# Kernel optimization log

Hardware: AMD Instinct MI355X
Metric: run time of the kernel (lower is better)

## Reference

```python
import jax, jax.numpy as jnp
import numpy as np
from jax import lax

H, HD, P, C, HID = 8, 64, 16, 512, 2048
ALIBI_ALPHA, START_I = 1.0, 0
EPS = 1e-5

def setup_inputs():
    key = jax.random.key(0)
    ks = jax.random.split(key, 20)
    s = 0.02
    return {
        "x": jax.random.normal(ks[0], (8, 1024, C), jnp.float32),
        "Wq": jax.random.normal(ks[1], (HD, HD), jnp.float32) * s,
        "Wk": jax.random.normal(ks[2], (HD, HD), jnp.float32) * s,
        "Wv": jax.random.normal(ks[3], (HD, HD), jnp.float32) * s,
        "Wo": jax.random.normal(ks[4], (C, C), jnp.float32) * s,
        "bo": jnp.zeros((C,), jnp.float32),
        "th_pre": jax.random.normal(ks[5], (H, H), jnp.float32) * (1.0 / np.sqrt(H)),
        "th_post": jax.random.normal(ks[6], (H, H), jnp.float32) * (1.0 / np.sqrt(H)),
        "p_keys": jax.random.normal(ks[7], (P, 1, HD), jnp.float32) * s,
        "p_values": jax.random.normal(ks[8], (P, 1, HD), jnp.float32) * s,
        "conv1_w": jax.random.normal(ks[9], (2 * HID, C, 3), jnp.float32) * s,
        "conv1_b": jnp.zeros((2 * HID,), jnp.float32),
        "conv2_w": jax.random.normal(ks[10], (C, HID, 3), jnp.float32) * s,
        "conv2_b": jnp.zeros((C,), jnp.float32),
        "ln1_g": jnp.ones((C,), jnp.float32),
        "ln1_b": jnp.zeros((C,), jnp.float32),
        "ln2_g": jnp.ones((C,), jnp.float32),
        "ln2_b": jnp.zeros((C,), jnp.float32),
    }

def _layernorm(x, g, b):
    mu = jnp.mean(x, axis=-1, keepdims=True)
    var = jnp.mean((x - mu) ** 2, axis=-1, keepdims=True)
    return (x - mu) * lax.rsqrt(var + EPS) * g + b

def _mha(x, Wq, Wk, Wv, Wo, bo, th_pre, th_post, p_keys, p_values):
    N, L, _ = x.shape
    xh = x.reshape(N, L, H, HD)
    q = xh @ Wq.T  # per-head-dim linear, as in torch (applied to last dim)
    k = xh @ Wk.T
    v = xh @ Wv.T
    # persistent memory: [P,1,HD] broadcast over batch and heads
    pk = jnp.broadcast_to(p_keys[None], (N, P, H, HD))
    pv = jnp.broadcast_to(p_values[None], (N, P, H, HD))
    k = jnp.concatenate([k, pk], axis=1)  # (N, L+P, H, HD)
    v = jnp.concatenate([v, pv], axis=1)
    energy = jnp.einsum('nqhd,nkhd->nhqk', q, k)
    # ALiBi: slope_h = 2^(-alpha*(h+1+start_i)), bias = -|q-k|*slope, zero on persistent cols
    slopes = 2.0 ** (-ALIBI_ALPHA * (jnp.arange(1, H + 1, dtype=jnp.float32) + START_I))
    t = jnp.arange(L, dtype=jnp.float32)
    dist = jnp.abs(t[:, None] - t[None, :])  # (L, L)
    bias = -dist[None, :, :] * slopes[:, None, None]  # (H, L, L)
    bias = jnp.pad(bias, ((0, 0), (0, 0), (0, P)))
    energy = energy + bias[None]
    energy = jnp.einsum('gh,nhqk->ngqk', th_pre, energy)  # pre-softmax talking heads (1x1 conv)
    attn = jax.nn.softmax(energy / jnp.sqrt(jnp.float32(C)), axis=-1)
    attn = jnp.einsum('gh,nhqk->ngqk', th_post, attn)  # post-softmax talking heads
    out = jnp.einsum('nhql,nlhd->nqhd', attn, v).reshape(N, L, C)
    return out @ Wo.T + bo

def _ffn(x, conv1_w, conv1_b, conv2_w, conv2_b):
    dn = ('NCH', 'OIH', 'NCH')
    xc = jnp.transpose(x, (0, 2, 1))  # (N, C, L)
    xp = jnp.pad(xc, ((0, 0), (0, 0), (1, 1)))  # same padding, k=3
    h = lax.conv_general_dilated(xp, conv1_w, (1,), 'VALID', dimension_numbers=dn) + conv1_b[None, :, None]
    h1, h2 = jnp.split(h, 2, axis=1)
    h = jax.nn.silu(h1) * h2  # swiglu
    hp = jnp.pad(h, ((0, 0), (0, 0), (1, 1)))
    y = lax.conv_general_dilated(hp, conv2_w, (1,), 'VALID', dimension_numbers=dn) + conv2_b[None, :, None]
    return jnp.transpose(y, (0, 2, 1))

def reference(x, Wq, Wk, Wv, Wo, bo, th_pre, th_post, p_keys, p_values,
              conv1_w, conv1_b, conv2_w, conv2_b, ln1_g, ln1_b, ln2_g, ln2_b):
    a = _mha(x, Wq, Wk, Wv, Wo, bo, th_pre, th_post, p_keys, p_values)
    x1 = _layernorm(a + x, ln1_g, ln1_b)
    f = _ffn(x1, conv1_w, conv1_b, conv2_w, conv2_b)
    return _layernorm(f + x1, ln2_g, ln2_b)
```

## Files before the change

kernel.cpp:

```cpp
#include <hip/hip_runtime.h>
#include <cstddef>
#include <cstdint>

#define NB   8
#define LQ   1024
#define CH   512
#define HHE  8
#define HDD  64
#define PPM  16
#define LP   1040
#define HID  2048

typedef unsigned short ushort_t;
typedef __attribute__((ext_vector_type(8))) short short8;
typedef __attribute__((ext_vector_type(4))) float floatx4;

static const size_t O_QB   = 0;
static const size_t O_KB   = 2097152;
static const size_t O_VB   = 4227072;
static const size_t O_VT   = 6356992;
static const size_t O_AOB  = 8486912;
static const size_t O_AF   = 10584064;
static const size_t O_X1B  = 16777216;
static const size_t O_HPAD = 18878464;
static const size_t O_W1   = 27283456;
static const size_t O_W2   = 30429184;
static const size_t O_WO   = 32002048;

__device__ __forceinline__ ushort_t f2bf(float f) {
  uint32_t u = __float_as_uint(f);
  u += 0x7FFFu + ((u >> 16) & 1u);
  return (ushort_t)(u >> 16);
}
__device__ __forceinline__ float bf2f(ushort_t h) {
  return __uint_as_float(((uint32_t)h) << 16);
}

__device__ __forceinline__ void async16(ushort_t* lds, const ushort_t* g) {
  __builtin_amdgcn_global_load_lds(
      (const __attribute__((address_space(1))) void*)g,
      (__attribute__((address_space(3))) void*)lds, 16, 0, 0);
}

__global__ __launch_bounds__(256) void pack_bf16_kernel(
    const float* __restrict__ src, ushort_t* __restrict__ dst,
    int K, int KD, int icShift)
{
  const int oc = blockIdx.x;
  const int icMask = (1 << icShift) - 1;
  for (int k = threadIdx.x; k < K; k += 256) {
    int ic = k & icMask, dl = k >> icShift;
    dst[(size_t)oc * K + k] = f2bf(src[(size_t)oc * K + ic * KD + dl]);
  }
}

template<int EPI>
__global__ __launch_bounds__(256, 2) void mfma_gemm(
    const ushort_t* __restrict__ Ab, const ushort_t* __restrict__ Bb,
    int K, int BS, int P, int NOUT,
    const float* __restrict__ bias, const float* __restrict__ res,
    float* __restrict__ outf, ushort_t* __restrict__ outh)
{
  __shared__ ushort_t As[128 * 32];
  __shared__ ushort_t Bs[128 * 32];
  const int t = threadIdx.x;
  const int w = t >> 6, l = t & 63;
  const int m0 = blockIdx.x * 128, n0 = blockIdx.y * 128;

  const int sub = l >> 2;
  const int kc8 = (l & 3) * 8;
  const ushort_t* aptr[2];
  const ushort_t* bptr[2];
  #pragma unroll
  for (int c = 0; c < 2; ++c) {
    int arow = m0 + w * 32 + c * 16 + sub;
    aptr[c] = Ab + (size_t)(arow >> 10) * BS + (size_t)(arow & 1023) * P + kc8;
    int brow = n0 + w * 32 + c * 16 + sub;
    bptr[c] = Bb + (size_t)brow * K + kc8;
  }

  const int wm = w >> 1, wn = w & 1;
  const int lm = l & 15, q = l >> 4;
  floatx4 acc[4][4];
  #pragma unroll
  for (int i = 0; i < 4; ++i)
    #pragma unroll
    for (int j = 0; j < 4; ++j)
      acc[i][j] = (floatx4){0.f, 0.f, 0.f, 0.f};

  const int kIters = K >> 5;
  for (int kt = 0; kt < kIters; ++kt) {
    __syncthreads();
    async16(&As[w * 1024 +   0], aptr[0]);
    async16(&As[w * 1024 + 512], aptr[1]);
    async16(&Bs[w * 1024 +   0], bptr[0]);
    async16(&Bs[w * 1024 + 512], bptr[1]);
    aptr[0] += 32; aptr[1] += 32; bptr[0] += 32; bptr[1] += 32;
    __syncthreads();
    short8 af[4], bf[4];
    #pragma unroll
    for (int i = 0; i < 4; ++i)
      af[i] = *(const short8*)&As[(wm * 64 + i * 16 + lm) * 32 + q * 8];
    #pragma unroll
    for (int i = 0; i < 4; ++i)
      bf[i] = *(const short8*)&Bs[(wn * 64 + i * 16 + lm) * 32 + q * 8];
    #pragma unroll
    for (int i = 0; i < 4; ++i)
      #pragma unroll
      for (int j = 0; j < 4; ++j)
        acc[i][j] = __builtin_amdgcn_mfma_f32_16x16x32_bf16(af[i], bf[j], acc[i][j], 0, 0, 0);
  }

  #pragma unroll
  for (int i = 0; i < 4; ++i) {
    #pragma unroll
    for (int j = 0; j < 4; ++j) {
      const int mbase = m0 + wm * 64 + i * 16 + q * 4;
      const int n = n0 + wn * 64 + j * 16 + lm;
      #pragma unroll
      for (int r = 0; r < 4; ++r) {
        const int m = mbase + r;
        float v = acc[i][j][r];
        if (EPI == 0) {
          outh[(size_t)m * NOUT + n] = f2bf(v);
        } else if (EPI == 1) {
          outf[(size_t)m * NOUT + n] = v + bias[n];
        } else {
          outf[(size_t)m * NOUT + n] = v + bias[n] + res[(size_t)m * NOUT + n];
        }
      }
    }
  }
}

__global__ __launch_bounds__(256) void qkv_mfma(
    const float* __restrict__ x,
    const float* __restrict__ Wq, const float* __restrict__ Wk, const float* __restrict__ Wv,
    ushort_t* __restrict__ qo, ushort_t* __restrict__ ko, ushort_t* __restrict__ vo)
{
  __shared__ ushort_t Ws[8 * 512];
  const int mat = blockIdx.y;
  const float* __restrict__ W = (mat == 0) ? Wq : (mat == 1) ? Wk : Wv;
  const int t = threadIdx.x;

  for (int e = t; e < 4096; e += 256) {
    const int oc = e >> 6, ic = e & 63;
    const int nt = oc >> 4, lmm = oc & 15, s = ic >> 5, qd = (ic >> 3) & 3, j = ic & 7;
    Ws[(((nt * 2 + s) * 4 + qd) * 16 + lmm) * 8 + j] = f2bf(W[e]);
  }

  const int w = t >> 6, l = t & 63;
  const int lm = l & 15, quad = l >> 4;
  const int tok0 = blockIdx.x * 64 + w * 16;

  short8 af[16];
  {
    const float* xrow = x + (size_t)(tok0 + lm) * CH + quad * 8;
    #pragma unroll
    for (int h = 0; h < 8; ++h) {
      #pragma unroll
      for (int s = 0; s < 2; ++s) {
        const float4 a = *(const float4*)(xrow + h * 64 + s * 32);
        const float4 b = *(const float4*)(xrow + h * 64 + s * 32 + 4);
        short8 f;
        f[0] = (short)f2bf(a.x); f[1] = (short)f2bf(a.y);
        f[2] = (short)f2bf(a.z); f[3] = (short)f2bf(a.w);
        f[4] = (short)f2bf(b.x); f[5] = (short)f2bf(b.y);
        f[6] = (short)f2bf(b.z); f[7] = (short)f2bf(b.w);
        af[h * 2 + s] = f;
      }
    }
  }
  __syncthreads();

  short8 bfr[8];
  #pragma unroll
  for (int nt = 0; nt < 4; ++nt)
    #pragma unroll
    for (int s = 0; s < 2; ++s)
      bfr[nt * 2 + s] = *(const short8*)&Ws[((nt * 2 + s) * 64 + l) * 8];

  const int n = tok0 >> 10, lpos = tok0 & 1023;
  ushort_t* outp;
  size_t base;
  if (mat == 0) { base = ((size_t)n * LQ + lpos) * CH; outp = qo; }
  else          { base = ((size_t)n * LP + lpos) * CH; outp = (mat == 1) ? ko : vo; }

  #pragma unroll
  for (int h = 0; h < 8; ++h) {
    floatx4 acc[4];
    #pragma unroll
    for (int nt = 0; nt < 4; ++nt) acc[nt] = (floatx4){0.f, 0.f, 0.f, 0.f};
    #pragma unroll
    for (int nt = 0; nt < 4; ++nt)
      #pragma unroll
      for (int s = 0; s < 2; ++s)
        acc[nt] = __builtin_amdgcn_mfma_f32_16x16x32_bf16(
            af[h * 2 + s], bfr[nt * 2 + s], acc[nt], 0, 0, 0);
    #pragma unroll
    for (int nt = 0; nt < 4; ++nt)
      #pragma unroll
      for (int r = 0; r < 4; ++r)
        outp[base + (size_t)(quad * 4 + r) * CH + h * 64 + nt * 16 + lm] =
            f2bf(acc[nt][r]);
  }
}

__global__ __launch_bounds__(256) void persist_kernel(
    const float* __restrict__ pk, const float* __restrict__ pv,
    ushort_t* __restrict__ ko, ushort_t* __restrict__ vo)
{
  const int t = blockIdx.x * 256 + threadIdx.x;
  const int n = t >> 13, p = (t >> 9) & 15, c = t & 511, d = c & 63;
  const size_t o = ((size_t)n * LP + LQ + p) * CH + c;
  ko[o] = f2bf(pk[p * 64 + d]);
  vo[o] = f2bf(pv[p * 64 + d]);
}

__global__ __launch_bounds__(256) void vtrans_kernel(
    const ushort_t* __restrict__ Vb, ushort_t* __restrict__ VT)
{
  __shared__ ushort_t Ls[16 * 520];
  const int n = blockIdx.y, k0 = blockIdx.x * 16;
  const int t = threadIdx.x;
  const int r = t >> 4;
  {
    const ushort_t* src = Vb + ((size_t)(n * LP + k0 + r)) * 512 + (t & 15) * 8;
    ushort_t* dst = &Ls[r * 520 + (t & 15) * 8];
    #pragma unroll
    for (int it = 0; it < 4; ++it)
      *(short8*)(dst + it * 128) = *(const short8*)(src + it * 128);
  }
  __syncthreads();
  #pragma unroll
  for (int rep = 0; rep < 2; ++rep) {
    const int d = t + rep * 256;
    short8 v0, v1;
    #pragma unroll
    for (int j = 0; j < 8; ++j) {
      v0[j] = (short)Ls[j * 520 + d];
      v1[j] = (short)Ls[(8 + j) * 520 + d];
    }
    ushort_t* dst = VT + ((size_t)(n * 512 + d)) * LP + k0;
    *(short8*)(dst)     = v0;
    *(short8*)(dst + 8) = v1;
  }
}

__global__ __launch_bounds__(256, 2) void attn_mfma(
    const ushort_t* __restrict__ Qb, const ushort_t* __restrict__ Kb,
    const ushort_t* __restrict__ VT,
    const float* __restrict__ thpre, const float* __restrict__ thpost,
    ushort_t* __restrict__ aob)
{
  __shared__ __align__(16) char smem[79872];
  ushort_t* Vt  = (ushort_t*)smem;
  float*    Ps  = (float*)(smem + 40960);
  float*    Eb0 = (float*)(smem + 59392);
  float*    Eb1 = (float*)(smem + 69632);
  float*    Ohn = (float*)smem;

  const int n = blockIdx.y, q0 = blockIdx.x * 16;
  const int t = threadIdx.x;
  const int w = t >> 6, l = t & 63;
  const int lm = l & 15, quad = l >> 4;
  const float invs = 0.044194173824159216f;

  short8 qf[4];
  {
    const ushort_t* qrow = Qb + ((size_t)(n * LQ + q0 + lm)) * 512 + (w * 2) * 64 + quad * 8;
    qf[0] = *(const short8*)(qrow);
    qf[1] = *(const short8*)(qrow + 32);
    qf[2] = *(const short8*)(qrow + 64);
    qf[3] = *(const short8*)(qrow + 96);
  }

  float tps[2][8], psl[2], tpo[2][8];
  #pragma unroll
  for (int gg = 0; gg < 2; ++gg) {
    const int g = w * 2 + gg;
    float ps = 0.f;
    #pragma unroll
    for (int h = 0; h < 8; ++h) {
      float tv = thpre[g * 8 + h] * invs;
      tps[gg][h] = tv;
      ps += tv * (1.0f / (float)(2 << h));
      tpo[gg][h] = thpost[g * 8 + h];
    }
    psl[gg] = ps;
  }

  float m_[2][4], z_[2][4];
  #pragma unroll
  for (int gg = 0; gg < 2; ++gg)
    #pragma unroll
    for (int r = 0; r < 4; ++r) { m_[gg][r] = -1e30f; z_[gg][r] = 0.f; }

  floatx4 o_[2][4];
  #pragma unroll
  for (int gg = 0; gg < 2; ++gg)
    #pragma unroll
    for (int ch = 0; ch < 4; ++ch) o_[gg][ch] = (floatx4){0.f, 0.f, 0.f, 0.f};

  const ushort_t* kg  = Kb + ((size_t)(n * LP + lm)) * 512 + (w * 2) * 64 + quad * 8;
  const ushort_t* vgA = VT + ((size_t)(n * 512) + t) * LP;
  const ushort_t* vgB = VT + ((size_t)(n * 512) + t + 256) * LP;

  short8 kfE[4], kfO[4], vX[4], vY[4];

  auto loadKg = [&](short8 (&r)[4], int step) {
    const ushort_t* p = kg + (size_t)step * 8192;
    r[0] = *(const short8*)(p);
    r[1] = *(const short8*)(p + 32);
    r[2] = *(const short8*)(p + 64);
    r[3] = *(const short8*)(p + 96);
  };
  auto loadVg = [&](short8 (&r)[4], int off) {
    r[0] = *(const short8*)(vgA + off); r[1] = *(const short8*)(vgA + off + 8);
    r[2] = *(const short8*)(vgB + off); r[3] = *(const short8*)(vgB + off + 8);
  };
  auto storeV = [&](short8 (&r)[4], int sub) {
    ushort_t* d0 = &Vt[(size_t)t * 40 + sub * 16];
    ushort_t* d1 = &Vt[(size_t)(t + 256) * 40 + sub * 16];
    *(short8*)(d0)     = r[0]; *(short8*)(d0 + 8) = r[1];
    *(short8*)(d1)     = r[2]; *(short8*)(d1 + 8) = r[3];
  };

  auto qktE = [&](short8 (&kf)[4], float* Eb) {
    #pragma unroll
    for (int hh = 0; hh < 2; ++hh) {
      floatx4 e = (floatx4){0.f, 0.f, 0.f, 0.f};
      e = __builtin_amdgcn_mfma_f32_16x16x32_bf16(qf[hh * 2 + 0], kf[hh * 2 + 0], e, 0, 0, 0);
      e = __builtin_amdgcn_mfma_f32_16x16x32_bf16(qf[hh * 2 + 1], kf[hh * 2 + 1], e, 0, 0, 0);
      *(floatx4*)&Eb[(((w * 2 + hh) * 16 + lm)) * 20 + quad * 4] = e;
    }
  };

  auto online2 = [&](int p) {
    float s0[2][4], s1[2][4];
    #pragma unroll
    for (int gg = 0; gg < 2; ++gg)
      #pragma unroll
      for (int r = 0; r < 4; ++r) { s0[gg][r] = 0.f; s1[gg][r] = 0.f; }
    #pragma unroll
    for (int h = 0; h < 8; ++h) {
      const floatx4 a = *(const floatx4*)&Eb0[(h * 16 + lm) * 20 + quad * 4];
      const floatx4 b = *(const floatx4*)&Eb1[(h * 16 + lm) * 20 + quad * 4];
      #pragma unroll
      for (int gg = 0; gg < 2; ++gg) {
        const float tv = tps[gg][h];
        #pragma unroll
        for (int r = 0; r < 4; ++r) {
          s0[gg][r] += tv * a[r];
          s1[gg][r] += tv * b[r];
        }
      }
    }
    const int k0 = 32 * p;
    float pm[2][4];
    #pragma unroll
    for (int r = 0; r < 4; ++r) {
      const float qpos = (float)(q0 + quad * 4 + r);
      const float d0 = fabsf(qpos - (float)(k0 + lm));
      const float d1 = fabsf(qpos - (float)(k0 + 16 + lm));
      #pragma unroll
      for (int gg = 0; gg < 2; ++gg) {
        s0[gg][r] -= d0 * psl[gg];
        s1[gg][r] -= d1 * psl[gg];
        pm[gg][r] = fmaxf(s0[gg][r], s1[gg][r]);
      }
    }
    #pragma unroll
    for (int off = 1; off < 16; off <<= 1)
      #pragma unroll
      for (int gg = 0; gg < 2; ++gg)
        #pragma unroll
        for (int r = 0; r < 4; ++r)
          pm[gg][r] = fmaxf(pm[gg][r], __shfl_xor(pm[gg][r], off));
    float sc[2][4];
    #pragma unroll
    for (int gg = 0; gg < 2; ++gg)
      #pragma unroll
      for (int r = 0; r < 4; ++r) {
        const float mn = fmaxf(m_[gg][r], pm[gg][r]);
        sc[gg][r] = __expf(m_[gg][r] - mn);
        const float p0 = __expf(s0[gg][r] - mn);
        const float p1 = __expf(s1[gg][r] - mn);
        z_[gg][r] = z_[gg][r] * sc[gg][r] + p0 + p1;
        m_[gg][r] = mn;
        float* prow = &Ps[((w * 2 + gg) * 16 + quad * 4 + r) * 36];
        prow[lm] = p0;
        prow[16 + lm] = p1;
      }
    #pragma unroll
    for (int gg = 0; gg < 2; ++gg)
      #pragma unroll
      for (int ch = 0; ch < 4; ++ch)
        #pragma unroll
        for (int r = 0; r < 4; ++r)
          o_[gg][ch][r] *= sc[gg][r];
  };

  auto online1 = [&]() {
    float s0[2][4];
    #pragma unroll
    for (int gg = 0; gg < 2; ++gg)
      #pragma unroll
      for (int r = 0; r < 4; ++r) s0[gg][r] = 0.f;
    #pragma unroll
    for (int h = 0; h < 8; ++h) {
      const floatx4 a = *(const floatx4*)&Eb0[(h * 16 + lm) * 20 + quad * 4];
      #pragma unroll
      for (int gg = 0; gg < 2; ++gg) {
        const float tv = tps[gg][h];
        #pragma unroll
        for (int r = 0; r < 4; ++r) s0[gg][r] += tv * a[r];
      }
    }
    float pm[2][4];
    #pragma unroll
    for (int gg = 0; gg < 2; ++gg)
      #pragma unroll
      for (int r = 0; r < 4; ++r) pm[gg][r] = s0[gg][r];
    #pragma unroll
    for (int off = 1; off < 16; off <<= 1)
      #pragma unroll
      for (int gg = 0; gg < 2; ++gg)
        #pragma unroll
        for (int r = 0; r < 4; ++r)
          pm[gg][r] = fmaxf(pm[gg][r], __shfl_xor(pm[gg][r], off));
    float sc[2][4];
    #pragma unroll
    for (int gg = 0; gg < 2; ++gg)
      #pragma unroll
      for (int r = 0; r < 4; ++r) {
        const float mn = fmaxf(m_[gg][r], pm[gg][r]);
        sc[gg][r] = __expf(m_[gg][r] - mn);
        const float p0 = __expf(s0[gg][r] - mn);
        z_[gg][r] = z_[gg][r] * sc[gg][r] + p0;
        m_[gg][r] = mn;
        float* prow = &Ps[((w * 2 + gg) * 16 + quad * 4 + r) * 36];
        prow[lm] = p0;
        prow[16 + lm] = 0.f;
      }
    #pragma unroll
    for (int gg = 0; gg < 2; ++gg)
      #pragma unroll
      for (int ch = 0; ch < 4; ++ch)
        #pragma unroll
        for (int r = 0; r < 4; ++r)
          o_[gg][ch][r] *= sc[gg][r];
  };

  auto pv = [&]() {
    #pragma unroll
    for (int gg = 0; gg < 2; ++gg) {
      const float4 pa = *(const float4*)&Ps[((w * 2 + gg) * 16 + lm) * 36 + quad * 8];
      const float4 pb = *(const float4*)&Ps[((w * 2 + gg) * 16 + lm) * 36 + quad * 8 + 4];
      short8 pk;
      pk[0] = (short)f2bf(pa.x); pk[1] = (short)f2bf(pa.y);
      pk[2] = (short)f2bf(pa.z); pk[3] = (short)f2bf(pa.w);
      pk[4] = (short)f2bf(pb.x); pk[5] = (short)f2bf(pb.y);
      pk[6] = (short)f2bf(pb.z); pk[7] = (short)f2bf(pb.w);
      #pragma unroll
      for (int ch = 0; ch < 4; ++ch) {
        const int d = (w * 2 + gg) * 64 + ch * 16 + lm;
        const short8 vf = *(const short8*)&Vt[d * 40 + quad * 8];
        o_[gg][ch] = __builtin_amdgcn_mfma_f32_16x16x32_bf16(pk, vf, o_[gg][ch], 0, 0, 0);
      }
    }
  };

  loadKg(kfE, 0);
  loadKg(kfO, 1);
  loadVg(vX, 0);
  loadVg(vY, 16);

  for (int p = 0; p < 32; ++p) {
    qktE(kfE, Eb0);
    qktE(kfO, Eb1);
    loadKg(kfE, 2 * p + 2);
    if (p < 31) loadKg(kfO, 2 * p + 3);
    __syncthreads();
    online2(p);
    storeV(vX, 0);
    storeV(vY, 1);
    loadVg(vX, 32 * (p + 1));
    if (p < 31) loadVg(vY, 32 * (p + 1) + 16);
    __syncthreads();
    pv();
  }
  qktE(kfE, Eb0);
  __syncthreads();
  online1();
  storeV(vX, 0);
  __syncthreads();
  pv();

  #pragma unroll
  for (int off = 1; off < 16; off <<= 1)
    #pragma unroll
    for (int gg = 0; gg < 2; ++gg)
      #pragma unroll
      for (int r = 0; r < 4; ++r)
        z_[gg][r] += __shfl_xor(z_[gg][r], off);
  #pragma unroll
  for (int gg = 0; gg < 2; ++gg)
    #pragma unroll
    for (int r = 0; r < 4; ++r) {
      const float zi = 1.0f / z_[gg][r];
      #pragma unroll
      for (int ch = 0; ch < 4; ++ch) o_[gg][ch][r] *= zi;
    }

  __syncthreads();
  #pragma unroll
  for (int gg = 0; gg < 2; ++gg)
    #pragma unroll
    for (int ch = 0; ch < 4; ++ch)
      #pragma unroll
      for (int r = 0; r < 4; ++r)
        Ohn[(w * 2 + gg) * 1088 + (quad * 4 + r) * 68 + ch * 16 + lm] = o_[gg][ch][r];
  __syncthreads();

  float acc[2][4][4];
  #pragma unroll
  for (int gg = 0; gg < 2; ++gg)
    #pragma unroll
    for (int ch = 0; ch < 4; ++ch)
      #pragma unroll
      for (int r = 0; r < 4; ++r) acc[gg][ch][r] = 0.f;
  #pragma unroll
  for (int h = 0; h < 8; ++h) {
    #pragma unroll
    for (int ch = 0; ch < 4; ++ch)
      #pragma unroll
      for (int r = 0; r < 4; ++r) {
        const float ov = Ohn[h * 1088 + (quad * 4 + r) * 68 + ch * 16 + lm];
        acc[0][ch][r] += tpo[0][h] * ov;
        acc[1][ch][r] += tpo[1][h] * ov;
      }
  }

  #pragma unroll
  for (int gg = 0; gg < 2; ++gg)
    #pragma unroll
    for (int ch = 0; ch < 4; ++ch) {
      const int d = (w * 2 + gg) * 64 + ch * 16 + lm;
      #pragma unroll
      for (int r = 0; r < 4; ++r)
        aob[((size_t)(n * LQ + q0 + quad * 4 + r)) * 512 + d] = f2bf(acc[gg][ch][r]);
    }
}

__global__ __launch_bounds__(256) void swiglu_kernel(
    const ushort_t* __restrict__ hraw, const float* __restrict__ bias,
    ushort_t* __restrict__ hpad)
{
  const int tok = blockIdx.x;
  const int n = tok >> 10, l = tok & 1023;
  const size_t src = (size_t)tok * 4096;
  const size_t dst = ((size_t)n * 1026 + l + 1) * 2048;
  for (int c = threadIdx.x; c < 2048; c += 256) {
    float h1 = bf2f(hraw[src + c]) + bias[c];
    float h2 = bf2f(hraw[src + 2048 + c]) + bias[2048 + c];
    float s = h1 / (1.f + __expf(-h1));
    hpad[dst + c] = f2bf(s * h2);
  }
}

__global__ __launch_bounds__(256) void zero_pads_kernel(
    ushort_t* __restrict__ x1b, ushort_t* __restrict__ hpad)
{
  const int b = blockIdx.x;
  const int n = b >> 1, side = b & 1;
  const size_t r = (size_t)n * 1026 + side * 1025;
  ushort2 z; z.x = 0; z.y = 0;
  *(ushort2*)&x1b[r * 512 + threadIdx.x * 2] = z;
  #pragma unroll
  for (int i = 0; i < 4; ++i)
    *(ushort2*)&hpad[r * 2048 + (threadIdx.x + 256 * i) * 2] = z;
}

__global__ __launch_bounds__(256) void ln_kernel(
    const float* __restrict__ in, const float* __restrict__ res,
    const float* __restrict__ g, const float* __restrict__ b,
    float* __restrict__ outp, ushort_t* __restrict__ bfout)
{
  const int w = threadIdx.x >> 6, lane = threadIdx.x & 63;
  const int tok = blockIdx.x * 4 + w;
  const size_t base = (size_t)tok * CH;
  float4 v0 = *(const float4*)&in[base + (lane << 2)];
  float4 v1 = *(const float4*)&in[base + 256 + (lane << 2)];
  if (res != nullptr) {
    float4 r0 = *(const float4*)&res[base + (lane << 2)];
    float4 r1 = *(const float4*)&res[base + 256 + (lane << 2)];
    v0.x += r0.x; v0.y += r0.y; v0.z += r0.z; v0.w += r0.w;
    v1.x += r1.x; v1.y += r1.y; v1.z += r1.z; v1.w += r1.w;
  }
  float s = v0.x + v0.y + v0.z + v0.w + v1.x + v1.y + v1.z + v1.w;
  #pragma unroll
  for (int off = 32; off > 0; off >>= 1) s += __shfl_xor(s, off);
  const float mu = s * (1.f / 512.f);
  float d0 = v0.x - mu, d1 = v0.y - mu, d2 = v0.z - mu, d3 = v0.w - mu;
  float d4 = v1.x - mu, d5 = v1.y - mu, d6 = v1.z - mu, d7 = v1.w - mu;
  float vs = d0*d0 + d1*d1 + d2*d2 + d3*d3 + d4*d4 + d5*d5 + d6*d6 + d7*d7;
  #pragma unroll
  for (int off = 32; off > 0; off >>= 1) vs += __shfl_xor(vs, off);
  const float r = rsqrtf(vs * (1.f / 512.f) + 1e-5f);
  float4 ga = *(const float4*)&g[(lane << 2)];
  float4 gb = *(const float4*)&g[256 + (lane << 2)];
  float4 ba = *(const float4*)&b[(lane << 2)];
  float4 bb = *(const float4*)&b[256 + (lane << 2)];
  float4 o0, o1;
  o0.x = d0 * r * ga.x + ba.x; o0.y = d1 * r * ga.y + ba.y;
  o0.z = d2 * r * ga.z + ba.z; o0.w = d3 * r * ga.w + ba.w;
  o1.x = d4 * r * gb.x + bb.x; o1.y = d5 * r * gb.y + bb.y;
  o1.z = d6 * r * gb.z + bb.z; o1.w = d7 * r * gb.w + bb.w;
  *(float4*)&outp[base + (lane << 2)] = o0;
  *(float4*)&outp[base + 256 + (lane << 2)] = o1;
  if (bfout != nullptr) {
    const int n = tok >> 10, ll = tok & 1023;
    const size_t bb2 = ((size_t)n * 1026 + ll + 1) * 512;
    ushort4 u0 = make_ushort4(f2bf(o0.x), f2bf(o0.y), f2bf(o0.z), f2bf(o0.w));
    ushort4 u1 = make_ushort4(f2bf(o1.x), f2bf(o1.y), f2bf(o1.z), f2bf(o1.w));
    *(ushort4*)&bfout[bb2 + (lane << 2)] = u0;
    *(ushort4*)&bfout[bb2 + 256 + (lane << 2)] = u1;
  }
}

extern "C" void kernel_launch(void* const* d_in, const int* in_sizes, int n_in,
                              void* d_out, int out_size, void* d_ws, size_t ws_size,
                              hipStream_t stream)
{
  (void)in_sizes; (void)n_in; (void)out_size; (void)ws_size;
  const float* x      = (const float*)d_in[0];
  const float* Wq     = (const float*)d_in[1];
  const float* Wk     = (const float*)d_in[2];
  const float* Wv     = (const float*)d_in[3];
  const float* Wo     = (const float*)d_in[4];
  const float* bo     = (const float*)d_in[5];
  const float* th_pre = (const float*)d_in[6];
  const float* th_post= (const float*)d_in[7];
  const float* p_keys = (const float*)d_in[8];
  const float* p_vals = (const float*)d_in[9];
  const float* c1w    = (const float*)d_in[10];
  const float* c1b    = (const float*)d_in[11];
  const float* c2w    = (const float*)d_in[12];
  const float* c2b    = (const float*)d_in[13];
  const float* ln1g   = (const float*)d_in[14];
  const float* ln1b   = (const float*)d_in[15];
  const float* ln2g   = (const float*)d_in[16];
  const float* ln2b   = (const float*)d_in[17];

  float* ws  = (float*)d_ws;
  float* out = (float*)d_out;

  ushort_t* Qb   = (ushort_t*)(ws + O_QB);
  ushort_t* Kb   = (ushort_t*)(ws + O_KB);
  ushort_t* Vb   = (ushort_t*)(ws + O_VB);
  ushort_t* VT   = (ushort_t*)(ws + O_VT);
  ushort_t* aob  = (ushort_t*)(ws + O_AOB);
  float*    abf  = ws + O_AF;
  float*    fbf  = abf;
  ushort_t* x1b  = (ushort_t*)(ws + O_X1B);
  ushort_t* hpad = (ushort_t*)(ws + O_HPAD);
  ushort_t* hraw = (ushort_t*)ws;
  ushort_t* w1p  = (ushort_t*)(ws + O_W1);
  ushort_t* w2p  = (ushort_t*)(ws + O_W2);
  ushort_t* wop  = (ushort_t*)(ws + O_WO);

  pack_bf16_kernel<<<4096, 256, 0, stream>>>(c1w, w1p, 1536, 3, 9);
  pack_bf16_kernel<<<512,  256, 0, stream>>>(c2w, w2p, 6144, 3, 11);
  pack_bf16_kernel<<<512,  256, 0, stream>>>(Wo,  wop, 512,  1, 9);

  qkv_mfma<<<dim3(128, 3), 256, 0, stream>>>(x, Wq, Wk, Wv, Qb, Kb, Vb);
  persist_kernel<<<256, 256, 0, stream>>>(p_keys, p_vals, Kb, Vb);
  vtrans_kernel<<<dim3(65, 8), 256, 0, stream>>>(Vb, VT);

  attn_mfma<<<dim3(64, 8), 256, 0, stream>>>(Qb, Kb, VT, th_pre, th_post, aob);

  mfma_gemm<2><<<dim3(64, 4), 256, 0, stream>>>(
      aob, wop, 512, 1024 * 512, 512, 512, bo, x, abf, nullptr);

  ln_kernel<<<2048, 256, 0, stream>>>(abf, nullptr, ln1g, ln1b, out, x1b);
  zero_pads_kernel<<<16, 256, 0, stream>>>(x1b, hpad);

  mfma_gemm<0><<<dim3(64, 32), 256, 0, stream>>>(
      x1b, w1p, 1536, 1026 * 512, 512, 4096, nullptr, nullptr, nullptr, hraw);

  swiglu_kernel<<<8192, 256, 0, stream>>>(hraw, c1b, hpad);

  mfma_gemm<1><<<dim3(64, 4), 256, 0, stream>>>(
      hpad, w2p, 6144, 1026 * 2048, 2048, 512, c2b, nullptr, fbf, nullptr);

  ln_kernel<<<2048, 256, 0, stream>>>(fbf, out, ln2g, ln2b, out, nullptr);
}
```

Measured before the change: 567.0 us.

## Split-K conv2 GEMM, stream V fragments from global in attention, vectorize swiglu

The second FFN GEMM (K=6144, only 256 blocks) is split four ways along K into partial fp32 buffers, and a new reduction kernel sums them and adds the bias. This raises parallelism on a grid that was too small to fill the GPU, at the cost of extra partial-sum traffic and one more launch. The attention kernel drops its LDS staging of V and loads MFMA V operands straight from the transposed global buffer into registers. That cuts LDS use and allows 3 blocks per CU. The swiglu kernel is vectorized to process 8 elements per thread with 16-byte loads and stores.

```diff
diff --git a/kernel.cpp b/kernel.cpp
--- a/kernel.cpp
+++ b/kernel.cpp
@@ -67,6 +67,9 @@
   const int w = t >> 6, l = t & 63;
   const int m0 = blockIdx.x * 128, n0 = blockIdx.y * 128;
 
+  const int kChunk = K / (int)gridDim.z;
+  const int kstart = blockIdx.z * kChunk;
+
   const int sub = l >> 2;
   const int kc8 = (l & 3) * 8;
   const ushort_t* aptr[2];
@@ -74,9 +77,9 @@
   #pragma unroll
   for (int c = 0; c < 2; ++c) {
     int arow = m0 + w * 32 + c * 16 + sub;
-    aptr[c] = Ab + (size_t)(arow >> 10) * BS + (size_t)(arow & 1023) * P + kc8;
+    aptr[c] = Ab + (size_t)(arow >> 10) * BS + (size_t)(arow & 1023) * P + kc8 + kstart;
     int brow = n0 + w * 32 + c * 16 + sub;
-    bptr[c] = Bb + (size_t)brow * K + kc8;
+    bptr[c] = Bb + (size_t)brow * K + kc8 + kstart;
   }
 
   const int wm = w >> 1, wn = w & 1;
@@ -88,7 +91,7 @@
     for (int j = 0; j < 4; ++j)
       acc[i][j] = (floatx4){0.f, 0.f, 0.f, 0.f};
 
-  const int kIters = K >> 5;
+  const int kIters = kChunk >> 5;
   for (int kt = 0; kt < kIters; ++kt) {
     __syncthreads();
     async16(&As[w * 1024 +   0], aptr[0]);
@@ -125,12 +128,32 @@
           outh[(size_t)m * NOUT + n] = f2bf(v);
         } else if (EPI == 1) {
           outf[(size_t)m * NOUT + n] = v + bias[n];
+        } else if (EPI == 2) {
+          outf[(size_t)m * NOUT + n] = v + bias[n] + res[(size_t)m * NOUT + n];
         } else {
-          outf[(size_t)m * NOUT + n] = v + bias[n] + res[(size_t)m * NOUT + n];
+          outf[(size_t)blockIdx.z * 4194304 + (size_t)m * NOUT + n] = v;
         }
       }
     }
   }
+}
+
+__global__ __launch_bounds__(256) void ksum_kernel(
+    float* __restrict__ pb, const float* __restrict__ bias)
+{
+  const size_t i = ((size_t)blockIdx.x * 256 + threadIdx.x) * 4;
+  float4 a = *(const float4*)&pb[i];
+  float4 b = *(const float4*)&pb[i +  4194304];
+  float4 c = *(const float4*)&pb[i +  8388608];
+  float4 d = *(const float4*)&pb[i + 12582912];
+  const int col = (int)(i & 511);
+  float4 bi = *(const float4*)&bias[col];
+  float4 o;
+  o.x = a.x + b.x + c.x + d.x + bi.x;
+  o.y = a.y + b.y + c.y + d.y + bi.y;
+  o.z = a.z + b.z + c.z + d.z + bi.z;
+  o.w = a.w + b.w + c.w + d.w + bi.w;
+  *(float4*)&pb[i] = o;
 }
 
 __global__ __launch_bounds__(256) void qkv_mfma(
@@ -247,18 +270,17 @@
   }
 }
 
-__global__ __launch_bounds__(256, 2) void attn_mfma(
+__global__ __launch_bounds__(256, 3) void attn_mfma(
     const ushort_t* __restrict__ Qb, const ushort_t* __restrict__ Kb,
     const ushort_t* __restrict__ VT,
     const float* __restrict__ thpre, const float* __restrict__ thpost,
     ushort_t* __restrict__ aob)
 {
-  __shared__ __align__(16) char smem[79872];
-  ushort_t* Vt  = (ushort_t*)smem;
-  float*    Ps  = (float*)(smem + 40960);
-  float*    Eb0 = (float*)(smem + 59392);
-  float*    Eb1 = (float*)(smem + 69632);
-  float*    Ohn = (float*)smem;
+  __shared__ __align__(16) char smem[38912];
+  float* Ps  = (float*)smem;
+  float* Eb0 = (float*)(smem + 18432);
+  float* Eb1 = (float*)(smem + 28672);
+  float* Ohn = (float*)smem;
 
   const int n = blockIdx.y, q0 = blockIdx.x * 16;
   const int t = threadIdx.x;
@@ -302,11 +324,11 @@
     #pragma unroll
     for (int ch = 0; ch < 4; ++ch) o_[gg][ch] = (floatx4){0.f, 0.f, 0.f, 0.f};
 
-  const ushort_t* kg  = Kb + ((size_t)(n * LP + lm)) * 512 + (w * 2) * 64 + quad * 8;
-  const ushort_t* vgA = VT + ((size_t)(n * 512) + t) * LP;
-  const ushort_t* vgB = VT + ((size_t)(n * 512) + t + 256) * LP;
-
-  short8 kfE[4], kfO[4], vX[4], vY[4];
+  const ushort_t* kg = Kb + ((size_t)(n * LP + lm)) * 512 + (w * 2) * 64 + quad * 8;
+  const ushort_t* vg0 = VT + ((size_t)(n * 512) + (w * 2 + 0) * 64 + lm) * LP;
+  const ushort_t* vg1 = VT + ((size_t)(n * 512) + (w * 2 + 1) * 64 + lm) * LP;
+
+  short8 kfE[4], kfO[4], vpf[8];
 
   auto loadKg = [&](short8 (&r)[4], int step) {
     const ushort_t* p = kg + (size_t)step * 8192;
@@ -315,15 +337,14 @@
     r[2] = *(const short8*)(p + 64);
     r[3] = *(const short8*)(p + 96);
   };
-  auto loadVg = [&](short8 (&r)[4], int off) {
-    r[0] = *(const short8*)(vgA + off); r[1] = *(const short8*)(vgA + off + 8);
-    r[2] = *(const short8*)(vgB + off); r[3] = *(const short8*)(vgB + off + 8);
-  };
-  auto storeV = [&](short8 (&r)[4], int sub) {
-    ushort_t* d0 = &Vt[(size_t)t * 40 + sub * 16];
-    ushort_t* d1 = &Vt[(size_t)(t + 256) * 40 + sub * 16];
-    *(short8*)(d0)     = r[0]; *(short8*)(d0 + 8) = r[1];
-    *(short8*)(d1)     = r[2]; *(short8*)(d1 + 8) = r[3];
+  auto loadV = [&](int p) {
+    int ko = 32 * p + quad * 8;
+    if (ko > 1032) ko = 1032;
+    #pragma unroll
+    for (int ch = 0; ch < 4; ++ch) {
+      vpf[ch]     = *(const short8*)(vg0 + (size_t)(ch * 16) * LP + ko);
+      vpf[4 + ch] = *(const short8*)(vg1 + (size_t)(ch * 16) * LP + ko);
+    }
   };
 
   auto qktE = [&](short8 (&kf)[4], float* Eb) {
@@ -463,18 +484,15 @@
       pk[4] = (short)f2bf(pb.x); pk[5] = (short)f2bf(pb.y);
       pk[6] = (short)f2bf(pb.z); pk[7] = (short)f2bf(pb.w);
       #pragma unroll
-      for (int ch = 0; ch < 4; ++ch) {
-        const int d = (w * 2 + gg) * 64 + ch * 16 + lm;
-        const short8 vf = *(const short8*)&Vt[d * 40 + quad * 8];
-        o_[gg][ch] = __builtin_amdgcn_mfma_f32_16x16x32_bf16(pk, vf, o_[gg][ch], 0, 0, 0);
-      }
+      for (int ch = 0; ch < 4; ++ch)
+        o_[gg][ch] = __builtin_amdgcn_mfma_f32_16x16x32_bf16(
+            pk, vpf[gg * 4 + ch], o_[gg][ch], 0, 0, 0);
     }
   };
 
   loadKg(kfE, 0);
   loadKg(kfO, 1);
-  loadVg(vX, 0);
-  loadVg(vY, 16);
+  loadV(0);
 
   for (int p = 0; p < 32; ++p) {
     qktE(kfE, Eb0);
@@ -483,17 +501,13 @@
     if (p < 31) loadKg(kfO, 2 * p + 3);
     __syncthreads();
     online2(p);
-    storeV(vX, 0);
-    storeV(vY, 1);
-    loadVg(vX, 32 * (p + 1));
-    if (p < 31) loadVg(vY, 32 * (p + 1) + 16);
     __syncthreads();
     pv();
+    loadV(p + 1);
   }
   qktE(kfE, Eb0);
   __syncthreads();
   online1();
-  storeV(vX, 0);
   __syncthreads();
   pv();
 
@@ -559,14 +573,26 @@
 {
   const int tok = blockIdx.x;
   const int n = tok >> 10, l = tok & 1023;
-  const size_t src = (size_t)tok * 4096;
-  const size_t dst = ((size_t)n * 1026 + l + 1) * 2048;
-  for (int c = threadIdx.x; c < 2048; c += 256) {
-    float h1 = bf2f(hraw[src + c]) + bias[c];
-    float h2 = bf2f(hraw[src + 2048 + c]) + bias[2048 + c];
-    float s = h1 / (1.f + __expf(-h1));
-    hpad[dst + c] = f2bf(s * h2);
-  }
+  const int c = threadIdx.x * 8;
+  const size_t src = (size_t)tok * 4096 + c;
+  const size_t dst = ((size_t)n * 1026 + l + 1) * 2048 + c;
+  const short8 h1v = *(const short8*)&hraw[src];
+  const short8 h2v = *(const short8*)&hraw[src + 2048];
+  const float4 b1a = *(const float4*)&bias[c];
+  const float4 b1b = *(const float4*)&bias[c + 4];
+  const float4 b2a = *(const float4*)&bias[2048 + c];
+  const float4 b2b = *(const float4*)&bias[2048 + c + 4];
+  const float bb1[8] = {b1a.x, b1a.y, b1a.z, b1a.w, b1b.x, b1b.y, b1b.z, b1b.w};
+  const float bb2[8] = {b2a.x, b2a.y, b2a.z, b2a.w, b2b.x, b2b.y, b2b.z, b2b.w};
+  short8 o;
+  #pragma unroll
+  for (int j = 0; j < 8; ++j) {
+    const float h1 = bf2f((ushort_t)h1v[j]) + bb1[j];
+    const float h2 = bf2f((ushort_t)h2v[j]) + bb2[j];
+    const float s = h1 / (1.f + __expf(-h1));
+    o[j] = (short)f2bf(s * h2);
+  }
+  *(short8*)&hpad[dst] = o;
 }
 
 __global__ __launch_bounds__(256) void zero_pads_kernel(
@@ -662,10 +688,10 @@
   ushort_t* VT   = (ushort_t*)(ws + O_VT);
   ushort_t* aob  = (ushort_t*)(ws + O_AOB);
   float*    abf  = ws + O_AF;
-  float*    fbf  = abf;
   ushort_t* x1b  = (ushort_t*)(ws + O_X1B);
   ushort_t* hpad = (ushort_t*)(ws + O_HPAD);
   ushort_t* hraw = (ushort_t*)ws;
+  float*    pk4  = ws;
   ushort_t* w1p  = (ushort_t*)(ws + O_W1);
   ushort_t* w2p  = (ushort_t*)(ws + O_W2);
   ushort_t* wop  = (ushort_t*)(ws + O_WO);
@@ -691,8 +717,9 @@
 
   swiglu_kernel<<<8192, 256, 0, stream>>>(hraw, c1b, hpad);
 
-  mfma_gemm<1><<<dim3(64, 4), 256, 0, stream>>>(
-      hpad, w2p, 6144, 1026 * 2048, 2048, 512, c2b, nullptr, fbf, nullptr);
-
-  ln_kernel<<<2048, 256, 0, stream>>>(fbf, out, ln2g, ln2b, out, nullptr);
-}
+  mfma_gemm<3><<<dim3(64, 4, 4), 256, 0, stream>>>(
+      hpad, w2p, 6144, 1026 * 2048, 2048, 512, nullptr, nullptr, pk4, nullptr);
+  ksum_kernel<<<4096, 256, 0, stream>>>(pk4, c2b);
+
+  ln_kernel<<<2048, 256, 0, stream>>>(pk4, out, ln2g, ln2b, out, nullptr);
+}
```

Result: slower. 931.0 us (+64.2%).
